# Kernel tuning notes

Measured on AMD Instinct MI355X. Metric: run time of the kernel, lower is better.

Reference implementation:

```python
import jax, jax.numpy as jnp
import numpy as np

N = 50000       # nodes
E = 1600000     # edges (avg degree 32)
D = 128         # in = hidden = out channels
H = 4           # attention heads


def setup_inputs() -> dict:
    key = jax.random.key(0)
    ks = jax.random.split(key, 9)
    s = 1.0 / np.sqrt(D)  # ~kaiming-scale linear weights
    return {
        "x": jax.random.normal(ks[0], (N, D), jnp.float32),
        "Wk": jax.random.normal(ks[1], (D, D), jnp.float32) * s,
        "bk": jnp.zeros((D,), jnp.float32),
        "Wq": jax.random.normal(ks[2], (D, D), jnp.float32) * s,
        "bq": jnp.zeros((D,), jnp.float32),
        "Wv": jax.random.normal(ks[3], (D, D), jnp.float32) * s,
        "bv": jnp.zeros((D,), jnp.float32),
        "src": jax.random.randint(ks[4], (E,), 0, N, dtype=jnp.int32),
        "dst": jax.random.randint(ks[5], (E,), 0, N, dtype=jnp.int32),
    }


def reference(x, Wk, bk, Wq, bq, Wv, bv, src, dst):
    n = x.shape[0]
    heads = H
    dk = Wk.shape[0] // heads
    dv = Wv.shape[0] // heads
    # Dense projections (near-roofline GEMMs)
    k = (x @ Wk.T + bk).reshape(n, heads, dk)
    q = (x @ Wq.T + bq).reshape(n, heads, dk)
    v = (x @ Wv.T + bv).reshape(n, heads, dv)
    # u_dot_v: per-edge per-head dot product (NO 1/sqrt(dk) scaling in source)
    scores = jnp.einsum('ehd,ehd->eh', k[src], q[dst])  # [E,H]
    # edge_softmax: softmax over incoming edges of each destination node
    m = jax.ops.segment_max(scores, dst, num_segments=n)        # [N,H]
    p = jnp.exp(scores - m[dst])                                 # [E,H]
    denom = jax.ops.segment_sum(p, dst, num_segments=n)         # [N,H]
    alpha = p / denom[dst]                                       # [E,H]
    # u_mul_e + sum: weighted scatter-aggregation of source values
    res = jax.ops.segment_sum(v[src] * alpha[:, :, None], dst, num_segments=n)  # [N,H,dv]
    # original: view(batch_size, -1, out_channels) with batch_size = N -> [N,1,out]
    return res.reshape(n, 1, heads * dv)
```

## Files before the change

kernel.cpp:

```cpp
#include <hip/hip_runtime.h>
#include <hip/hip_bf16.h>
#include <hip/hip_fp16.h>

#define NN 50000
#define NE 1600000
#define DD 128
#define HH 4
#define BSH2 5
#define NBKT2 1563
#define NBP2 2048
#define CAP 1408
#define PCHUNK 8192
#define NPB 196
#define GB 512

typedef __attribute__((ext_vector_type(8))) short short8;
typedef __attribute__((ext_vector_type(4))) float floatx4;
typedef __attribute__((ext_vector_type(2))) _Float16 h2;

__device__ inline h2 as_h2(unsigned u) {
    union { unsigned u; h2 h; } c; c.u = u; return c.h;
}

__device__ inline float dot4(h2 a01, h2 a23, h2 b01, h2 b23) {
#if defined(__has_builtin) && __has_builtin(__builtin_amdgcn_fdot2)
    return __builtin_amdgcn_fdot2(a01, b01, __builtin_amdgcn_fdot2(a23, b23, 0.f, false), false);
#else
    return (float)a01.x * (float)b01.x + (float)a01.y * (float)b01.y +
           (float)a23.x * (float)b23.x + (float)a23.y * (float)b23.y;
#endif
}

__global__ __launch_bounds__(256) void prep_w(
    const float* __restrict__ Wk, const float* __restrict__ Wq, const float* __restrict__ Wv,
    unsigned short* __restrict__ hi, unsigned short* __restrict__ lo, int* __restrict__ bcur)
{
    int j = blockIdx.x * 256 + threadIdx.x;
    if (j < NBP2) bcur[j] = 0;
    if (j >= 3 * DD * DD) return;
    int which = j / (DD * DD);
    int off = j - which * (DD * DD);
    const float* W = (which == 0) ? Wk : (which == 1) ? Wq : Wv;
    float w = W[off];
    unsigned int b = __float_as_uint(w);
    unsigned short h = (unsigned short)(b >> 16);
    float hf = __uint_as_float((unsigned int)h << 16);
    float l = w - hf;
    hi[j] = h;
    lo[j] = (unsigned short)(__float_as_uint(l) >> 16);
}

__global__ __launch_bounds__(256) void part(
    const int* __restrict__ src, const int* __restrict__ dst,
    int* __restrict__ bcur, int* __restrict__ epack)
{
    __shared__ int h[NBP2];
    __shared__ int c2[NBP2];
    int pb = blockIdx.x;
    int b0 = pb * PCHUNK;
    int n = min(PCHUNK, NE - b0);
    for (int i = threadIdx.x; i < NBP2; i += 256) h[i] = 0;
    __syncthreads();
    for (int i = threadIdx.x; i < n; i += 256)
        atomicAdd(&h[dst[b0 + i] >> BSH2], 1);
    __syncthreads();
    for (int i = threadIdx.x; i < NBP2; i += 256)
        c2[i] = h[i] ? i * CAP + atomicAdd(&bcur[i], h[i]) : 0;
    __syncthreads();
    for (int i = threadIdx.x; i < n; i += 256) {
        int d = dst[b0 + i];
        int s = src[b0 + i];
        int bkt = d >> BSH2;
        int pos = atomicAdd(&c2[bkt], 1);
        if (pos < (bkt + 1) * CAP)
            epack[pos] = ((d & 31) << 16) | s;
    }
}

__global__ __launch_bounds__(256) void gemm(
    const float* __restrict__ x,
    const unsigned short* __restrict__ whi, const unsigned short* __restrict__ wlo,
    const float* __restrict__ bk, const float* __restrict__ bq, const float* __restrict__ bv,
    uint2* __restrict__ kv2, uint4* __restrict__ qh4)
{
    __shared__ __align__(16) unsigned char smem[81920];

    uint4* wh4 = (uint4*)smem;
    uint4* wl4 = (uint4*)(smem + 32768);
    int tid = threadIdx.x;
    int wave = tid >> 6, lane = tid & 63;
    int m = lane & 15, quad = lane >> 4;
    unsigned short* st = (unsigned short*)(smem + 65536 + wave * 4096);
    uint4* st4 = (uint4*)st;
    uint2* st2 = (uint2*)st;

    for (int pp = 0; pp < 3; ++pp) {
        int wm = (pp == 0) ? 0 : (pp == 1) ? 2 : 1;
        const uint4* gh = (const uint4*)whi + (size_t)wm * 2048;
        const uint4* gl = (const uint4*)wlo + (size_t)wm * 2048;
        __syncthreads();
        for (int g = tid; g < 2048; g += 256) {
            int l = (g & ~15) | ((g ^ (g >> 4)) & 15);
            wh4[l] = gh[g];
            wl4[l] = gl[g];
        }
        __syncthreads();
        const float* bias = (pp == 0) ? bk : (pp == 1) ? bv : bq;
        float bs[8];
#pragma unroll
        for (int ct = 0; ct < 8; ++ct) bs[ct] = bias[ct * 16 + m];

        for (int tile = blockIdx.x * 4 + wave; tile < 3125; tile += GB * 4) {
            int n0 = tile * 16;
            const float* xrow = x + (size_t)(n0 + m) * DD + quad * 8;
            short8 ah[4], al[4];
#pragma unroll
            for (int ks = 0; ks < 4; ++ks) {
                const float* xr = xrow + ks * 32;
                float4 t0 = *(const float4*)xr;
                float4 t1 = *(const float4*)(xr + 4);
                float xv[8] = {t0.x, t0.y, t0.z, t0.w, t1.x, t1.y, t1.z, t1.w};
#pragma unroll
                for (int j = 0; j < 8; ++j) {
                    unsigned int b = __float_as_uint(xv[j]);
                    unsigned short h = (unsigned short)(b >> 16);
                    float hf = __uint_as_float((unsigned int)h << 16);
                    float l = xv[j] - hf;
                    ah[ks][j] = (short)h;
                    al[ks][j] = (short)(__float_as_uint(l) >> 16);
                }
            }

            floatx4 acc[8];
#pragma unroll
            for (int ct = 0; ct < 8; ++ct) acc[ct] = (floatx4){0.f, 0.f, 0.f, 0.f};

#pragma unroll
            for (int ks = 0; ks < 4; ++ks) {
#pragma unroll
                for (int ct = 0; ct < 8; ++ct) {
                    int r = ct * 16 + m;
                    int idx = r * 16 + ((ks * 4 + quad) ^ m);
                    short8 bh = ((const short8*)wh4)[idx];
                    short8 bl = ((const short8*)wl4)[idx];
                    acc[ct] = __builtin_amdgcn_mfma_f32_16x16x32_bf16(ah[ks], bh, acc[ct], 0, 0, 0);
                    acc[ct] = __builtin_amdgcn_mfma_f32_16x16x32_bf16(ah[ks], bl, acc[ct], 0, 0, 0);
                    acc[ct] = __builtin_amdgcn_mfma_f32_16x16x32_bf16(al[ks], bh, acc[ct], 0, 0, 0);
                }
            }

#pragma unroll
            for (int ct = 0; ct < 8; ++ct) {
                int j = ct * 16 + m;
#pragma unroll
                for (int r = 0; r < 4; ++r)
                    st[(quad * 4 + r) * 128 + j] = __half_as_ushort(__float2half(acc[ct][r] + bs[ct]));
            }
            if (pp < 2) {
                int voff = (pp == 1) ? 1 : 0;
#pragma unroll
                for (int t = 0; t < 8; ++t) {
                    int flat = t * 64 + lane;
                    int row = flat >> 5, gg = flat & 31;
                    kv2[((size_t)(n0 + row)) * 64 + gg * 2 + voff] = st2[flat];
                }
            } else {
#pragma unroll
                for (int t = 0; t < 4; ++t) {
                    int flat = t * 64 + lane;
                    qh4[((size_t)(n0 + (flat >> 4))) * 16 + (flat & 15)] = st4[flat];
                }
            }
        }
    }
}

__global__ __launch_bounds__(256) void gat_bucket(
    const __half* __restrict__ qh, const uint4* __restrict__ kvpack,
    const int* __restrict__ epack, const int* __restrict__ bcur,
    float* __restrict__ out)
{
    __shared__ int hist[32];
    __shared__ int cur[32];
    __shared__ int begs[33];
    __shared__ unsigned short els[CAP];
    int b = blockIdx.x;
    int cnt = min(bcur[b], CAP);
    int base = b * CAP;
    int n0 = b << BSH2;
    int nnodes = min(32, NN - n0);
    int tid = threadIdx.x;

    if (tid < 32) hist[tid] = 0;
    __syncthreads();
    for (int e = tid; e < cnt; e += 256)
        atomicAdd(&hist[epack[base + e] >> 16], 1);
    __syncthreads();
    if (tid < 32) {
        int c = hist[tid], inc = c;
#pragma unroll
        for (int d = 1; d < 32; d <<= 1) {
            int t = __shfl_up(inc, d);
            if (tid >= d) inc += t;
        }
        int excl = inc - c;
        begs[tid] = excl;
        cur[tid]  = excl;
        if (tid == 31) begs[32] = excl + c;
    }
    __syncthreads();
    for (int e = tid; e < cnt; e += 256) {
        int p = epack[base + e];
        int pos = atomicAdd(&cur[p >> 16], 1);
        els[pos] = (unsigned short)(p & 0xFFFF);
    }
    __syncthreads();

    int il = tid & 31;
    int hw = tid >> 5;
    const uint4* kvb = kvpack + il;

    for (int nl = hw; nl < nnodes; nl += 8) {
        int node = n0 + nl;
        int beg = begs[nl], end = begs[nl + 1];

        uint2 qq = *(const uint2*)(qh + (size_t)node * 128 + il * 4);
        h2 qh01 = as_h2(qq.x), qh23 = as_h2(qq.y);

        float m = -INFINITY, ssum = 0.f;
        float o0 = 0.f, o1 = 0.f, o2 = 0.f, o3 = 0.f;

        uint4 kvv[8];
        int nh = end - beg; if (nh > 8) nh = 8;
        if (nh > 0) {
#pragma unroll
            for (int i = 0; i < 8; ++i) {
                int s = els[beg + ((i < nh) ? i : 0)];
                kvv[i] = kvb[(size_t)s * 32];
            }
        }

        for (int j = beg; j < end; j += 8) {
            int jn = j + 8;
            int rem = end - jn;
            uint4 kvn[8];
            if (rem > 0) {
                int nhc = (rem > 8) ? 8 : rem;
#pragma unroll
                for (int i = 0; i < 8; ++i) {
                    int s = els[jn + ((i < nhc) ? i : 0)];
                    kvn[i] = kvb[(size_t)s * 32];
                }
            }
            float p[8];
#pragma unroll
            for (int i = 0; i < 8; ++i) {
                float t = dot4(as_h2(kvv[i].x), as_h2(kvv[i].y), qh01, qh23);
                t += __shfl_xor(t, 1);
                t += __shfl_xor(t, 2);
                t += __shfl_xor(t, 4);
                p[i] = (i < nh) ? t : -INFINITY;
            }
            float gm = fmaxf(fmaxf(fmaxf(p[0], p[1]), fmaxf(p[2], p[3])),
                             fmaxf(fmaxf(p[4], p[5]), fmaxf(p[6], p[7])));
            float nm = fmaxf(m, gm);
            float nmc = fmaxf(nm, -1e30f);
            float scale = __expf(m - nmc);
            ssum *= scale; o0 *= scale; o1 *= scale; o2 *= scale; o3 *= scale;
#pragma unroll
            for (int i = 0; i < 8; ++i) {
                float w = __expf(p[i] - nmc);
                ssum += w;
                o0 += w * (float)as_h2(kvv[i].z).x;
                o1 += w * (float)as_h2(kvv[i].z).y;
                o2 += w * (float)as_h2(kvv[i].w).x;
                o3 += w * (float)as_h2(kvv[i].w).y;
            }
            m = nm;
#pragma unroll
            for (int i = 0; i < 8; ++i) kvv[i] = kvn[i];
            nh = (rem > 8) ? 8 : rem;
        }

        float invd = (ssum > 0.f) ? 1.f / ssum : 0.f;
        float4 r = {o0 * invd, o1 * invd, o2 * invd, o3 * invd};
        *(float4*)(out + (size_t)node * DD + il * 4) = r;
    }
}

extern "C" void kernel_launch(void* const* d_in, const int* in_sizes, int n_in,
                              void* d_out, int out_size, void* d_ws, size_t ws_size,
                              hipStream_t stream) {
    const float* x  = (const float*)d_in[0];
    const float* Wk = (const float*)d_in[1];
    const float* bk = (const float*)d_in[2];
    const float* Wq = (const float*)d_in[3];
    const float* bq = (const float*)d_in[4];
    const float* Wv = (const float*)d_in[5];
    const float* bv = (const float*)d_in[6];
    const int* src = (const int*)d_in[7];
    const int* dst = (const int*)d_in[8];

    uint4*  kvpack = (uint4*)d_ws;
    __half* qh     = (__half*)(kvpack + (size_t)NN * 32);
    unsigned short* whi = (unsigned short*)(qh + (size_t)NN * DD);
    unsigned short* wlo = whi + (size_t)3 * DD * DD;
    int* epack = (int*)(wlo + (size_t)3 * DD * DD);
    int* bcur  = epack + (size_t)NBKT2 * CAP;

    prep_w<<<192, 256, 0, stream>>>(Wk, Wq, Wv, whi, wlo, bcur);
    part<<<NPB, 256, 0, stream>>>(src, dst, bcur, epack);
    gemm<<<GB, 256, 0, stream>>>(x, whi, wlo, bk, bq, bv, (uint2*)kvpack, (uint4*)qh);
    gat_bucket<<<NBKT2, 256, 0, stream>>>(qh, kvpack, epack, bcur, (float*)d_out);
}
```

Before: 294.5 us.

## Split K/V layout, triple-buffer gathers, and fuse weight prep into partition kernel

The per-node K and V halves now sit in separate contiguous 256-byte blocks instead of interleaved 16-byte chunks, and the GEMM epilogue writes this layout. The aggregation loop moves from double-buffered to triple-buffered gathers of 8-edge chunks to keep more loads in flight, and sets a launch-bounds occupancy hint. Weight splitting is merged into the partition kernel as extra blocks, and bucket-counter zeroing moves to a memset, removing one kernel launch. The deeper prefetch uses more registers, which can lower occupancy, and each edge now needs two 8-byte loads where it used to need one 16-byte load.

```diff
diff --git a/kernel.cpp b/kernel.cpp
--- a/kernel.cpp
+++ b/kernel.cpp
@@ -12,6 +12,7 @@
 #define CAP 1408
 #define PCHUNK 8192
 #define NPB 196
+#define WSB 192
 #define GB 512
 
 typedef __attribute__((ext_vector_type(8))) short short8;
@@ -31,31 +32,28 @@
 #endif
 }
 
-__global__ __launch_bounds__(256) void prep_w(
+__global__ __launch_bounds__(256) void part_prep(
     const float* __restrict__ Wk, const float* __restrict__ Wq, const float* __restrict__ Wv,
-    unsigned short* __restrict__ hi, unsigned short* __restrict__ lo, int* __restrict__ bcur)
-{
-    int j = blockIdx.x * 256 + threadIdx.x;
-    if (j < NBP2) bcur[j] = 0;
-    if (j >= 3 * DD * DD) return;
-    int which = j / (DD * DD);
-    int off = j - which * (DD * DD);
-    const float* W = (which == 0) ? Wk : (which == 1) ? Wq : Wv;
-    float w = W[off];
-    unsigned int b = __float_as_uint(w);
-    unsigned short h = (unsigned short)(b >> 16);
-    float hf = __uint_as_float((unsigned int)h << 16);
-    float l = w - hf;
-    hi[j] = h;
-    lo[j] = (unsigned short)(__float_as_uint(l) >> 16);
-}
-
-__global__ __launch_bounds__(256) void part(
+    unsigned short* __restrict__ hi, unsigned short* __restrict__ lo,
     const int* __restrict__ src, const int* __restrict__ dst,
     int* __restrict__ bcur, int* __restrict__ epack)
 {
     __shared__ int h[NBP2];
     __shared__ int c2[NBP2];
+    if (blockIdx.x >= NPB) {
+        int j = (blockIdx.x - NPB) * 256 + threadIdx.x;
+        int which = j / (DD * DD);
+        int off = j - which * (DD * DD);
+        const float* W = (which == 0) ? Wk : (which == 1) ? Wq : Wv;
+        float w = W[off];
+        unsigned int b = __float_as_uint(w);
+        unsigned short hh = (unsigned short)(b >> 16);
+        float hf = __uint_as_float((unsigned int)hh << 16);
+        float l = w - hf;
+        hi[j] = hh;
+        lo[j] = (unsigned short)(__float_as_uint(l) >> 16);
+        return;
+    }
     int pb = blockIdx.x;
     int b0 = pb * PCHUNK;
     int n = min(PCHUNK, NE - b0);
@@ -157,12 +155,12 @@
                     st[(quad * 4 + r) * 128 + j] = __half_as_ushort(__float2half(acc[ct][r] + bs[ct]));
             }
             if (pp < 2) {
-                int voff = (pp == 1) ? 1 : 0;
+                int voff = (pp == 1) ? 32 : 0;
 #pragma unroll
                 for (int t = 0; t < 8; ++t) {
                     int flat = t * 64 + lane;
                     int row = flat >> 5, gg = flat & 31;
-                    kv2[((size_t)(n0 + row)) * 64 + gg * 2 + voff] = st2[flat];
+                    kv2[((size_t)(n0 + row)) * 64 + voff + gg] = st2[flat];
                 }
             } else {
 #pragma unroll
@@ -175,8 +173,53 @@
     }
 }
 
-__global__ __launch_bounds__(256) void gat_bucket(
-    const __half* __restrict__ qh, const uint4* __restrict__ kvpack,
+#define GAT_ISSUE(c, K, V)                                              \
+    do {                                                                \
+        if ((c) < nch) {                                                \
+            int base_ = beg + (c) * 8;                                  \
+            int nh_ = cnt - (c) * 8; if (nh_ > 8) nh_ = 8;              \
+            _Pragma("unroll")                                           \
+            for (int i_ = 0; i_ < 8; ++i_) {                            \
+                int s_ = els[base_ + ((i_ < nh_) ? i_ : 0)];            \
+                const uint2* p_ = kv2 + (size_t)s_ * 64 + il;           \
+                K[i_] = p_[0];                                          \
+                V[i_] = p_[32];                                         \
+            }                                                           \
+        }                                                               \
+    } while (0)
+
+#define GAT_COMPUTE(c, K, V)                                            \
+    do {                                                                \
+        int nh_ = cnt - (c) * 8; if (nh_ > 8) nh_ = 8;                  \
+        float p_[8];                                                    \
+        _Pragma("unroll")                                               \
+        for (int i_ = 0; i_ < 8; ++i_) {                                \
+            float t_ = dot4(as_h2(K[i_].x), as_h2(K[i_].y), qh01, qh23);\
+            t_ += __shfl_xor(t_, 1);                                    \
+            t_ += __shfl_xor(t_, 2);                                    \
+            t_ += __shfl_xor(t_, 4);                                    \
+            p_[i_] = (i_ < nh_) ? t_ : -INFINITY;                       \
+        }                                                               \
+        float gm_ = fmaxf(fmaxf(fmaxf(p_[0], p_[1]), fmaxf(p_[2], p_[3])), \
+                          fmaxf(fmaxf(p_[4], p_[5]), fmaxf(p_[6], p_[7]))); \
+        float nm_ = fmaxf(m, gm_);                                      \
+        float nmc_ = fmaxf(nm_, -1e30f);                                \
+        float sc_ = __expf(m - nmc_);                                   \
+        ssum *= sc_; o0 *= sc_; o1 *= sc_; o2 *= sc_; o3 *= sc_;        \
+        _Pragma("unroll")                                               \
+        for (int i_ = 0; i_ < 8; ++i_) {                                \
+            float w_ = __expf(p_[i_] - nmc_);                           \
+            ssum += w_;                                                 \
+            o0 += w_ * (float)as_h2(V[i_].x).x;                         \
+            o1 += w_ * (float)as_h2(V[i_].x).y;                         \
+            o2 += w_ * (float)as_h2(V[i_].y).x;                         \
+            o3 += w_ * (float)as_h2(V[i_].y).y;                         \
+        }                                                               \
+        m = nm_;                                                        \
+    } while (0)
+
+__global__ __launch_bounds__(256, 4) void gat_bucket(
+    const __half* __restrict__ qh, const uint2* __restrict__ kv2,
     const int* __restrict__ epack, const int* __restrict__ bcur,
     float* __restrict__ out)
 {
@@ -185,7 +228,7 @@
     __shared__ int begs[33];
     __shared__ unsigned short els[CAP];
     int b = blockIdx.x;
-    int cnt = min(bcur[b], CAP);
+    int ecnt = min(bcur[b], CAP);
     int base = b * CAP;
     int n0 = b << BSH2;
     int nnodes = min(32, NN - n0);
@@ -193,7 +236,7 @@
 
     if (tid < 32) hist[tid] = 0;
     __syncthreads();
-    for (int e = tid; e < cnt; e += 256)
+    for (int e = tid; e < ecnt; e += 256)
         atomicAdd(&hist[epack[base + e] >> 16], 1);
     __syncthreads();
     if (tid < 32) {
@@ -209,7 +252,7 @@
         if (tid == 31) begs[32] = excl + c;
     }
     __syncthreads();
-    for (int e = tid; e < cnt; e += 256) {
+    for (int e = tid; e < ecnt; e += 256) {
         int p = epack[base + e];
         int pos = atomicAdd(&cur[p >> 16], 1);
         els[pos] = (unsigned short)(p & 0xFFFF);
@@ -218,11 +261,11 @@
 
     int il = tid & 31;
     int hw = tid >> 5;
-    const uint4* kvb = kvpack + il;
 
     for (int nl = hw; nl < nnodes; nl += 8) {
         int node = n0 + nl;
-        int beg = begs[nl], end = begs[nl + 1];
+        int beg = begs[nl];
+        int cnt = begs[nl + 1] - beg;
 
         uint2 qq = *(const uint2*)(qh + (size_t)node * 128 + il * 4);
         h2 qh01 = as_h2(qq.x), qh23 = as_h2(qq.y);
@@ -230,56 +273,24 @@
         float m = -INFINITY, ssum = 0.f;
         float o0 = 0.f, o1 = 0.f, o2 = 0.f, o3 = 0.f;
 
-        uint4 kvv[8];
-        int nh = end - beg; if (nh > 8) nh = 8;
-        if (nh > 0) {
-#pragma unroll
-            for (int i = 0; i < 8; ++i) {
-                int s = els[beg + ((i < nh) ? i : 0)];
-                kvv[i] = kvb[(size_t)s * 32];
-            }
-        }
-
-        for (int j = beg; j < end; j += 8) {
-            int jn = j + 8;
-            int rem = end - jn;
-            uint4 kvn[8];
-            if (rem > 0) {
-                int nhc = (rem > 8) ? 8 : rem;
-#pragma unroll
-                for (int i = 0; i < 8; ++i) {
-                    int s = els[jn + ((i < nhc) ? i : 0)];
-                    kvn[i] = kvb[(size_t)s * 32];
-                }
-            }
-            float p[8];
-#pragma unroll
-            for (int i = 0; i < 8; ++i) {
-                float t = dot4(as_h2(kvv[i].x), as_h2(kvv[i].y), qh01, qh23);
-                t += __shfl_xor(t, 1);
-                t += __shfl_xor(t, 2);
-                t += __shfl_xor(t, 4);
-                p[i] = (i < nh) ? t : -INFINITY;
-            }
-            float gm = fmaxf(fmaxf(fmaxf(p[0], p[1]), fmaxf(p[2], p[3])),
-                             fmaxf(fmaxf(p[4], p[5]), fmaxf(p[6], p[7])));
-            float nm = fmaxf(m, gm);
-            float nmc = fmaxf(nm, -1e30f);
-            float scale = __expf(m - nmc);
-            ssum *= scale; o0 *= scale; o1 *= scale; o2 *= scale; o3 *= scale;
-#pragma unroll
-            for (int i = 0; i < 8; ++i) {
-                float w = __expf(p[i] - nmc);
-                ssum += w;
-                o0 += w * (float)as_h2(kvv[i].z).x;
-                o1 += w * (float)as_h2(kvv[i].z).y;
-                o2 += w * (float)as_h2(kvv[i].w).x;
-                o3 += w * (float)as_h2(kvv[i].w).y;
-            }
-            m = nm;
-#pragma unroll
-            for (int i = 0; i < 8; ++i) kvv[i] = kvn[i];
-            nh = (rem > 8) ? 8 : rem;
+        if (cnt > 0) {
+            int nch = (cnt + 7) >> 3;
+            uint2 kA[8], vA[8], kB[8], vB[8], kC[8], vC[8];
+            GAT_ISSUE(0, kA, vA);
+            GAT_ISSUE(1, kB, vB);
+            GAT_ISSUE(2, kC, vC);
+            int j = 0;
+            for (;;) {
+                GAT_COMPUTE(j, kA, vA);
+                if (++j >= nch) break;
+                GAT_ISSUE(j + 2, kA, vA);
+                GAT_COMPUTE(j, kB, vB);
+                if (++j >= nch) break;
+                GAT_ISSUE(j + 2, kB, vB);
+                GAT_COMPUTE(j, kC, vC);
+                if (++j >= nch) break;
+                GAT_ISSUE(j + 2, kC, vC);
+            }
         }
 
         float invd = (ssum > 0.f) ? 1.f / ssum : 0.f;
@@ -301,15 +312,15 @@
     const int* src = (const int*)d_in[7];
     const int* dst = (const int*)d_in[8];
 
-    uint4*  kvpack = (uint4*)d_ws;
-    __half* qh     = (__half*)(kvpack + (size_t)NN * 32);
+    uint2*  kv2 = (uint2*)d_ws;
+    __half* qh  = (__half*)(kv2 + (size_t)NN * 64);
     unsigned short* whi = (unsigned short*)(qh + (size_t)NN * DD);
     unsigned short* wlo = whi + (size_t)3 * DD * DD;
     int* epack = (int*)(wlo + (size_t)3 * DD * DD);
     int* bcur  = epack + (size_t)NBKT2 * CAP;
 
-    prep_w<<<192, 256, 0, stream>>>(Wk, Wq, Wv, whi, wlo, bcur);
-    part<<<NPB, 256, 0, stream>>>(src, dst, bcur, epack);
-    gemm<<<GB, 256, 0, stream>>>(x, whi, wlo, bk, bq, bv, (uint2*)kvpack, (uint4*)qh);
-    gat_bucket<<<NBKT2, 256, 0, stream>>>(qh, kvpack, epack, bcur, (float*)d_out);
-}
+    hipMemsetAsync(bcur, 0, NBP2 * sizeof(int), stream);
+    part_prep<<<NPB + WSB, 256, 0, stream>>>(Wk, Wq, Wv, whi, wlo, src, dst, bcur, epack);
+    gemm<<<GB, 256, 0, stream>>>(x, whi, wlo, bk, bq, bv, kv2, (uint4*)qh);
+    gat_bucket<<<NBKT2, 256, 0, stream>>>(qh, kv2, epack, bcur, (float*)d_out);
+}
```

After: 475.0 us. +61.3%, slower.
